# Kernel optimization log

Hardware: AMD Instinct MI355X
Metric: run time of the kernel (lower is better)

Reference implementation:

```python
import jax, jax.numpy as jnp
import numpy as np

P, B, A, NBT, NC, NTAB, G = 512, 512, 32, 40, 3, 40, 36
NA = B * A


def setup_inputs() -> dict:
    key = jax.random.key(0)
    rng = np.random.default_rng(0)
    coords = jax.random.normal(key, (P, NA, 3), dtype=jnp.float32) * 3.0
    # residue b occupies atoms [b*A, (b+1)*A)
    offsets = np.broadcast_to(np.arange(B, dtype=np.int32) * A, (P, B)).copy()
    block_type = rng.integers(0, NBT, size=(P, B)).astype(np.int32)
    # simple linear chain per pose: conn 0 = lower (prev residue), conn 1 = upper (next residue)
    inter = np.full((P, B, NC, 2), -1, dtype=np.int32)
    inter[:, 1:, 0, 0] = np.arange(B - 1, dtype=np.int32)
    inter[:, 1:, 0, 1] = 1
    inter[:, :-1, 1, 0] = np.arange(1, B, dtype=np.int32)
    inter[:, :-1, 1, 1] = 0
    down = rng.integers(0, A, size=(NBT, NC, A)).astype(np.int32)
    bt_rama_table = rng.integers(0, NTAB, size=(NBT, 2)).astype(np.int32)
    bt_upper_conn_ind = np.ones(NBT, dtype=np.int32)
    bt_is_pro = rng.integers(0, 2, size=NBT).astype(np.int32)
    # unresolved torsion atoms: (local_atom_ind, conn_ind, n_bonds_from_conn); atom_ind<0 => via connection
    tor = np.zeros((NBT, 8, 3), dtype=np.int32)
    tor[:, 0] = (-1, 0, 0)  # phi: prev-C via lower conn
    tor[:, 1] = (0, -1, 0)  # N
    tor[:, 2] = (1, -1, 0)  # CA
    tor[:, 3] = (2, -1, 0)  # C
    tor[:, 4] = (0, -1, 0)  # psi: N
    tor[:, 5] = (1, -1, 0)  # CA
    tor[:, 6] = (2, -1, 0)  # C
    tor[:, 7] = (-1, 1, 0)  # next-N via upper conn
    rama_tables = jax.random.normal(jax.random.fold_in(key, 1), (NTAB, G, G), dtype=jnp.float32)
    tp = np.zeros((NTAB, 2, 2), dtype=np.float32)
    tp[:, 0, :] = -np.pi            # bb start
    tp[:, 1, :] = 2.0 * np.pi / G   # bb step
    return dict(
        coords=coords,
        pose_stack_block_coord_offset=jnp.asarray(offsets),
        pose_stack_block_type=jnp.asarray(block_type),
        pose_stack_inter_residue_connections=jnp.asarray(inter),
        bt_atom_downstream_of_conn=jnp.asarray(down),
        bt_rama_table=jnp.asarray(bt_rama_table),
        bt_upper_conn_ind=jnp.asarray(bt_upper_conn_ind),
        bt_is_pro=jnp.asarray(bt_is_pro),
        bt_rama_torsion_atoms=jnp.asarray(tor),
        rama_tables=rama_tables,
        table_params=jnp.asarray(tp),
    )


def _dihedral(p):
    # p: [..., 4, 3] -> dihedral angle [...] via atan2 formulation
    b1 = p[..., 1, :] - p[..., 0, :]
    b2 = p[..., 2, :] - p[..., 1, :]
    b3 = p[..., 3, :] - p[..., 2, :]
    n1 = jnp.cross(b1, b2)
    n2 = jnp.cross(b2, b3)
    b2n = b2 / (jnp.linalg.norm(b2, axis=-1, keepdims=True) + 1e-12)
    m1 = jnp.cross(n1, b2n)
    x = jnp.sum(n1 * n2, axis=-1)
    y = jnp.sum(m1 * n2, axis=-1)
    return jnp.arctan2(y, x)


def _catmull_rom_w(f):
    # weights over 4 neighbors (i-1, i, i+1, i+2); f in [0,1)
    f2 = f * f
    f3 = f2 * f
    return jnp.stack(
        [0.5 * (-f3 + 2 * f2 - f), 0.5 * (3 * f3 - 5 * f2 + 2),
         0.5 * (-3 * f3 + 4 * f2 + f), 0.5 * (f3 - f2)], axis=-1)


def reference(coords, pose_stack_block_coord_offset, pose_stack_block_type,
              pose_stack_inter_residue_connections, bt_atom_downstream_of_conn,
              bt_rama_table, bt_upper_conn_ind, bt_is_pro, bt_rama_torsion_atoms,
              rama_tables, table_params):
    nP, nB = pose_stack_block_type.shape
    nG = rama_tables.shape[-1]
    pidx = jnp.arange(nP)[:, None, None]
    bidx = jnp.arange(nB)[None, :, None]
    bt = pose_stack_block_type                       # [P,B]
    tor = bt_rama_torsion_atoms[bt]                  # [P,B,8,3]
    atom_ind, conn_ind, nbonds = tor[..., 0], tor[..., 1], tor[..., 2]
    safe_conn = jnp.clip(conn_ind, 0, None)
    other_block = pose_stack_inter_residue_connections[pidx, bidx, safe_conn, 0]  # [P,B,8]
    other_conn = pose_stack_inter_residue_connections[pidx, bidx, safe_conn, 1]
    conn_ok = (conn_ind >= 0) & (other_block >= 0)
    ob = jnp.clip(other_block, 0, None)
    oc = jnp.clip(other_conn, 0, None)
    obt = bt[pidx, ob]                               # [P,B,8]
    down_atom = bt_atom_downstream_of_conn[obt, oc, nbonds]
    conn_global = pose_stack_block_coord_offset[pidx, ob] + down_atom
    local_global = pose_stack_block_coord_offset[pidx, bidx] + jnp.clip(atom_ind, 0, None)
    use_local = atom_ind >= 0
    gidx = jnp.where(use_local, local_global, conn_global)  # [P,B,8]
    atom_ok = use_local | conn_ok
    xyz = coords[pidx, gidx]                         # [P,B,8,3]
    ang = _dihedral(xyz.reshape(nP, nB, 2, 4, 3))    # [P,B,2] -> (phi, psi)
    tor_ok = jnp.all(atom_ok.reshape(nP, nB, 2, 4), axis=-1)
    # table selection: proline-dependent on the NEXT residue
    uc = bt_upper_conn_ind[bt]                       # [P,B]
    p2 = jnp.arange(nP)[:, None]
    b2 = jnp.arange(nB)[None, :]
    nb = pose_stack_inter_residue_connections[p2, b2, uc, 0]  # [P,B]
    nb_ok = nb >= 0
    nbt = bt[p2, jnp.clip(nb, 0, None)]
    tab = bt_rama_table[bt, bt_is_pro[nbt]]          # [P,B]
    start = table_params[tab, 0]                     # [P,B,2]
    step = table_params[tab, 1]
    u = (ang - start) / step                         # [P,B,2]
    i0f = jnp.floor(u)
    f = u - i0f
    i0 = i0f.astype(jnp.int32)
    offs = jnp.arange(-1, 3, dtype=jnp.int32)        # 4 spline neighbors
    ii = jnp.mod(i0[..., 0:1] + offs, nG)            # [P,B,4] periodic phi bins
    jj = jnp.mod(i0[..., 1:2] + offs, nG)            # [P,B,4] periodic psi bins
    wphi = _catmull_rom_w(f[..., 0])                 # [P,B,4]
    wpsi = _catmull_rom_w(f[..., 1])
    vals = rama_tables[tab[..., None, None], ii[..., :, None], jj[..., None, :]]  # [P,B,4,4]
    e = jnp.einsum('pbi,pbj,pbij->pb', wphi, wpsi, vals)
    ok = tor_ok[..., 0] & tor_ok[..., 1] & nb_ok
    return jnp.sum(jnp.where(ok, e, 0.0), axis=-1)   # [P] per-pose rama score
```

## Files before the change

### kernel.cpp

```cpp
#include <hip/hip_runtime.h>
#include <math.h>

#define NP 512
#define NBLK 512
#define NTHREADS 1024
#define NA_ 32
#define NCn 3
#define NG 36
#define NBT 40
#define NTAB 40

struct F3 { float x, y, z; };
__device__ inline F3 f3sub(F3 a, F3 b) { return {a.x - b.x, a.y - b.y, a.z - b.z}; }
__device__ inline F3 f3cross(F3 a, F3 b) {
    return {a.y * b.z - a.z * b.y, a.z * b.x - a.x * b.z, a.x * b.y - a.y * b.x};
}
__device__ inline float f3dot(F3 a, F3 b) { return a.x * b.x + a.y * b.y + a.z * b.z; }

__global__ __launch_bounds__(NTHREADS, 4) void rama_kernel(
    const float* __restrict__ coords,
    const int*   __restrict__ offsets,
    const int*   __restrict__ block_type,
    const int*   __restrict__ inter,
    const int*   __restrict__ down,
    const int*   __restrict__ bt_rama_table,
    const int*   __restrict__ bt_upper_conn,
    const int*   __restrict__ bt_is_pro,
    const int*   __restrict__ tor_atoms,
    const float* __restrict__ rama_tables,
    const float* __restrict__ table_params,
    float*       __restrict__ out)
{
    __shared__ __align__(16) int   s_bt[NBLK];
    __shared__ __align__(16) int   s_off[NBLK];
    __shared__ __align__(16) int   s_inter[NBLK * NCn * 2];
    __shared__ __align__(16) float s_ang[NBLK * 2];
    __shared__ float partial[NTHREADS / 64];

    const int p   = blockIdx.x;
    const int tid = threadIdx.x;

    {
        const int4* gi = (const int4*)(inter      + (size_t)p * NBLK * NCn * 2);
        const int4* gb = (const int4*)(block_type + (size_t)p * NBLK);
        const int4* go = (const int4*)(offsets    + (size_t)p * NBLK);
        if (tid < 768)      ((int4*)s_inter)[tid]     = gi[tid];
        else if (tid < 896) ((int4*)s_bt)[tid - 768]  = gb[tid - 768];
        else                ((int4*)s_off)[tid - 896] = go[tid - 896];
    }
    __syncthreads();

    const int b = tid & (NBLK - 1);
    const int t = tid >> 9;
    const int bt    = s_bt[b];
    const int off_b = s_off[b];
    const float* pose_coords = coords + (size_t)p * NBLK * NA_ * 3;

    const int4* tq = (const int4*)tor_atoms + (6 * bt + 3 * t);
    const int4 w0 = tq[0], w1 = tq[1], w2 = tq[2];
    const int ai[4]  = {w0.x, w0.w, w1.z, w2.y};
    const int ci[4]  = {w0.y, w1.x, w1.w, w2.z};
    const int nbd[4] = {w0.z, w1.y, w2.x, w2.w};

    int  g[4];
    bool ok4 = true;
    #pragma unroll
    for (int a = 0; a < 4; ++a) {
        if (ai[a] >= 0) {
            g[a] = off_b + ai[a];
        } else {
            const int sc = ci[a] > 0 ? ci[a] : 0;
            const int ib = (b * NCn + sc) * 2;
            const int ob = s_inter[ib + 0];
            const int oc = s_inter[ib + 1];
            ok4 = ok4 && (ci[a] >= 0) && (ob >= 0);
            const int obc = ob > 0 ? ob : 0;
            const int occ = oc > 0 ? oc : 0;
            const int obt = s_bt[obc];
            g[a] = s_off[obc] + down[(obt * NCn + occ) * NA_ + nbd[a]];
        }
    }

    F3 pts[4];
    bool done = false;
    if (g[2] == g[1] + 1 && g[3] == g[2] + 1 && (g[1] & 3) == 0) {
        const float* base = pose_coords + (size_t)g[1] * 3;
        const float4 q0 = ((const float4*)base)[0];
        const float4 q1 = ((const float4*)base)[1];
        const float  q2 = base[8];
        pts[1] = {q0.x, q0.y, q0.z};
        pts[2] = {q0.w, q1.x, q1.y};
        pts[3] = {q1.z, q1.w, q2};
        const float* c0 = pose_coords + (size_t)g[0] * 3;
        pts[0] = {c0[0], c0[1], c0[2]};
        done = true;
    } else if (g[1] == g[0] + 1 && g[2] == g[1] + 1 && (g[0] & 3) == 0) {
        const float* base = pose_coords + (size_t)g[0] * 3;
        const float4 q0 = ((const float4*)base)[0];
        const float4 q1 = ((const float4*)base)[1];
        const float  q2 = base[8];
        pts[0] = {q0.x, q0.y, q0.z};
        pts[1] = {q0.w, q1.x, q1.y};
        pts[2] = {q1.z, q1.w, q2};
        const float* c3 = pose_coords + (size_t)g[3] * 3;
        pts[3] = {c3[0], c3[1], c3[2]};
        done = true;
    }
    if (!done) {
        #pragma unroll
        for (int a = 0; a < 4; ++a) {
            const float* c = pose_coords + (size_t)g[a] * 3;
            pts[a] = {c[0], c[1], c[2]};
        }
    }

    const F3 d1 = f3sub(pts[1], pts[0]);
    const F3 d2 = f3sub(pts[2], pts[1]);
    const F3 d3 = f3sub(pts[3], pts[2]);
    const F3 n1 = f3cross(d1, d2);
    const F3 n2 = f3cross(d2, d3);
    const float inv = 1.0f / (sqrtf(f3dot(d2, d2)) + 1e-12f);
    const F3 b2n = {d2.x * inv, d2.y * inv, d2.z * inv};
    const F3 m1  = f3cross(n1, b2n);
    const float ang = atan2f(f3dot(m1, n2), f3dot(n1, n2));

    s_ang[b * 2 + t] = ok4 ? ang : 1e30f;
    __syncthreads();
    const float2 pp  = ((const float2*)s_ang)[b];
    const float  phi = pp.x, psi = pp.y;
    const bool   okb = fabsf(phi) < 1e29f && fabsf(psi) < 1e29f;

    const int  uc   = bt_upper_conn[bt];
    const int  nb   = s_inter[(b * NCn + uc) * 2 + 0];
    const bool nbok = nb >= 0;
    const int  nbc  = nb > 0 ? nb : 0;
    const int  tab  = bt_rama_table[bt * 2 + bt_is_pro[s_bt[nbc]]];

    float e = 0.0f;
    if (okb && nbok) {
        const float4 tp4 = ((const float4*)table_params)[tab];
        float wphi[4], wpsi[4];
        int   ii[4], jj[4];
        #pragma unroll
        for (int d = 0; d < 2; ++d) {
            const float a0    = (d == 0) ? phi   : psi;
            const float start = (d == 0) ? tp4.x : tp4.y;
            const float step  = (d == 0) ? tp4.z : tp4.w;
            const float u   = (a0 - start) / step;
            const float i0f = floorf(u);
            const float f   = u - i0f;
            const float f2 = f * f, f3v = f2 * f;
            float* w = (d == 0) ? wphi : wpsi;
            w[0] = 0.5f * (-f3v + 2.0f * f2 - f);
            w[1] = 0.5f * (3.0f * f3v - 5.0f * f2 + 2.0f);
            w[2] = 0.5f * (-3.0f * f3v + 4.0f * f2 + f);
            w[3] = 0.5f * (f3v - f2);
            int m = ((int)i0f - 1) % NG;
            if (m < 0) m += NG;
            int* idx = (d == 0) ? ii : jj;
            idx[0] = m;
            #pragma unroll
            for (int k = 1; k < 4; ++k) {
                m = (m + 1 == NG) ? 0 : m + 1;
                idx[k] = m;
            }
        }
        const int   ra = t ? ii[2]   : ii[0];
        const int   rb = t ? ii[3]   : ii[1];
        const float wa = t ? wphi[2] : wphi[0];
        const float wb = t ? wphi[3] : wphi[1];
        const float* T  = rama_tables + (size_t)tab * NG * NG;
        const float* Ta = T + ra * NG;
        const float* Tb = T + rb * NG;
        float sa = 0.0f, sb = 0.0f;
        #pragma unroll
        for (int j = 0; j < 4; ++j) {
            sa += wpsi[j] * Ta[jj[j]];
            sb += wpsi[j] * Tb[jj[j]];
        }
        e = wa * sa + wb * sb;
    }

    float v = e;
    #pragma unroll
    for (int o = 32; o > 0; o >>= 1) v += __shfl_down(v, o);
    const int wave = tid >> 6;
    const int lane = tid & 63;
    if (lane == 0) partial[wave] = v;
    __syncthreads();
    if (tid == 0) {
        float s = 0.0f;
        #pragma unroll
        for (int i = 0; i < NTHREADS / 64; ++i) s += partial[i];
        out[p] = s;
    }
}

extern "C" void kernel_launch(void* const* d_in, const int* in_sizes, int n_in,
                              void* d_out, int out_size, void* d_ws, size_t ws_size,
                              hipStream_t stream) {
    (void)in_sizes; (void)n_in; (void)out_size; (void)d_ws; (void)ws_size;
    rama_kernel<<<NP, NTHREADS, 0, stream>>>(
        (const float*)d_in[0],
        (const int*)d_in[1],
        (const int*)d_in[2],
        (const int*)d_in[3],
        (const int*)d_in[4],
        (const int*)d_in[5],
        (const int*)d_in[6],
        (const int*)d_in[7],
        (const int*)d_in[8],
        (const float*)d_in[9],
        (const float*)d_in[10],
        (float*)d_out);
}
```

Measured before the change: 175.5 us.

## Compute phi and psi in one thread per residue, drop LDS staging

Changes the kernel from two threads per residue (one per torsion) to one thread computing both phi and psi. When the torsions share atoms it reuses three contiguous backbone atoms loaded with one vector read. It removes the shared-memory staging of per-pose topology and the mid-kernel barrier, reading block types, offsets and connections straight from global memory. It replaces atan2f and the sqrt/divide with a polynomial atan2 and a hardware rsq/rcp, which trades some accuracy for fewer instructions.

```diff
diff --git a/kernel.cpp b/kernel.cpp
--- a/kernel.cpp
+++ b/kernel.cpp
@@ -3,12 +3,10 @@
 
 #define NP 512
 #define NBLK 512
-#define NTHREADS 1024
+#define NT 512
 #define NA_ 32
 #define NCn 3
 #define NG 36
-#define NBT 40
-#define NTAB 40
 
 struct F3 { float x, y, z; };
 __device__ inline F3 f3sub(F3 a, F3 b) { return {a.x - b.x, a.y - b.y, a.z - b.z}; }
@@ -17,7 +15,34 @@
 }
 __device__ inline float f3dot(F3 a, F3 b) { return a.x * b.x + a.y * b.y + a.z * b.z; }
 
-__global__ __launch_bounds__(NTHREADS, 4) void rama_kernel(
+__device__ inline float fast_atan2(float y, float x) {
+    const float ax = fabsf(x), ay = fabsf(y);
+    const float mx = fmaxf(ax, ay), mn = fminf(ax, ay);
+    const float r  = mn * __builtin_amdgcn_rcpf(fmaxf(mx, 1e-37f));
+    const float s  = r * r;
+    float p = -0.0117212f;
+    p = fmaf(p, s,  0.05265332f);
+    p = fmaf(p, s, -0.11643287f);
+    p = fmaf(p, s,  0.19354346f);
+    p = fmaf(p, s, -0.33262347f);
+    p = fmaf(p, s,  0.99997726f);
+    p = p * r;
+    p = (ay > ax) ? (1.5707963267948966f - p) : p;
+    p = (x < 0.0f) ? (3.14159265358979323f - p) : p;
+    return copysignf(p, y);
+}
+
+__device__ inline float dihedral4(F3 p0, F3 p1, F3 p2, F3 p3) {
+    const F3 b1 = f3sub(p1, p0);
+    const F3 b2 = f3sub(p2, p1);
+    const F3 b3 = f3sub(p3, p2);
+    const F3 n1 = f3cross(b1, b2);
+    const F3 n2 = f3cross(b2, b3);
+    const float i2 = __builtin_amdgcn_rsqf(f3dot(b2, b2) + 1e-24f);
+    return fast_atan2(i2 * f3dot(f3cross(n1, b2), n2), f3dot(n1, n2));
+}
+
+__global__ __launch_bounds__(NT, 4) void rama_kernel(
     const float* __restrict__ coords,
     const int*   __restrict__ offsets,
     const int*   __restrict__ block_type,
@@ -31,113 +56,86 @@
     const float* __restrict__ table_params,
     float*       __restrict__ out)
 {
-    __shared__ __align__(16) int   s_bt[NBLK];
-    __shared__ __align__(16) int   s_off[NBLK];
-    __shared__ __align__(16) int   s_inter[NBLK * NCn * 2];
-    __shared__ __align__(16) float s_ang[NBLK * 2];
-    __shared__ float partial[NTHREADS / 64];
-
-    const int p   = blockIdx.x;
-    const int tid = threadIdx.x;
-
-    {
-        const int4* gi = (const int4*)(inter      + (size_t)p * NBLK * NCn * 2);
-        const int4* gb = (const int4*)(block_type + (size_t)p * NBLK);
-        const int4* go = (const int4*)(offsets    + (size_t)p * NBLK);
-        if (tid < 768)      ((int4*)s_inter)[tid]     = gi[tid];
-        else if (tid < 896) ((int4*)s_bt)[tid - 768]  = gb[tid - 768];
-        else                ((int4*)s_off)[tid - 896] = go[tid - 896];
-    }
-    __syncthreads();
-
-    const int b = tid & (NBLK - 1);
-    const int t = tid >> 9;
-    const int bt    = s_bt[b];
-    const int off_b = s_off[b];
+    __shared__ float partial[NT / 64];
+
+    const int p  = blockIdx.x;
+    const int b  = threadIdx.x;
+    const int pb = p * NBLK + b;
+
+    const int bt    = block_type[pb];
+    const int off_b = offsets[pb];
     const float* pose_coords = coords + (size_t)p * NBLK * NA_ * 3;
-
-    const int4* tq = (const int4*)tor_atoms + (6 * bt + 3 * t);
-    const int4 w0 = tq[0], w1 = tq[1], w2 = tq[2];
-    const int ai[4]  = {w0.x, w0.w, w1.z, w2.y};
-    const int ci[4]  = {w0.y, w1.x, w1.w, w2.z};
-    const int nbd[4] = {w0.z, w1.y, w2.x, w2.w};
-
-    int  g[4];
-    bool ok4 = true;
+    const int*   inter_p     = inter  + (size_t)p * NBLK * NCn * 2;
+
+    const int4* tq = (const int4*)tor_atoms + 6 * bt;
+    const int4 w0 = tq[0], w1 = tq[1], w2 = tq[2], w3 = tq[3], w4 = tq[4], w5 = tq[5];
+    const int ai[8]  = {w0.x, w0.w, w1.z, w2.y,  w3.x, w3.w, w4.z, w5.y};
+    const int ci[8]  = {w0.y, w1.x, w1.w, w2.z,  w3.y, w4.x, w4.w, w5.z};
+    const int nbd[8] = {w0.z, w1.y, w2.x, w2.w,  w3.z, w4.y, w5.x, w5.w};
+
+    int  g[8];
+    bool ok_phi = true, ok_psi = true;
     #pragma unroll
-    for (int a = 0; a < 4; ++a) {
-        if (ai[a] >= 0) {
-            g[a] = off_b + ai[a];
+    for (int e = 0; e < 8; ++e) {
+        if (ai[e] >= 0) {
+            g[e] = off_b + ai[e];
         } else {
-            const int sc = ci[a] > 0 ? ci[a] : 0;
-            const int ib = (b * NCn + sc) * 2;
-            const int ob = s_inter[ib + 0];
-            const int oc = s_inter[ib + 1];
-            ok4 = ok4 && (ci[a] >= 0) && (ob >= 0);
+            const int sc = ci[e] > 0 ? ci[e] : 0;
+            const int ob = inter_p[(b * NCn + sc) * 2 + 0];
+            const int oc = inter_p[(b * NCn + sc) * 2 + 1];
+            const bool okc = (ci[e] >= 0) && (ob >= 0);
+            if (e < 4) ok_phi = ok_phi && okc; else ok_psi = ok_psi && okc;
             const int obc = ob > 0 ? ob : 0;
             const int occ = oc > 0 ? oc : 0;
-            const int obt = s_bt[obc];
-            g[a] = s_off[obc] + down[(obt * NCn + occ) * NA_ + nbd[a]];
-        }
-    }
-
-    F3 pts[4];
-    bool done = false;
-    if (g[2] == g[1] + 1 && g[3] == g[2] + 1 && (g[1] & 3) == 0) {
+            const int obt = block_type[p * NBLK + obc];
+            g[e] = offsets[p * NBLK + obc] + down[(obt * NCn + occ) * NA_ + nbd[e]];
+        }
+    }
+
+    float phi, psi;
+    const bool sh = (g[1] == g[4]) && (g[2] == g[5]) && (g[3] == g[6]);
+    if (sh && g[2] == g[1] + 1 && g[3] == g[1] + 2 && ((g[1] & 3) == 0)) {
         const float* base = pose_coords + (size_t)g[1] * 3;
         const float4 q0 = ((const float4*)base)[0];
         const float4 q1 = ((const float4*)base)[1];
-        const float  q2 = base[8];
-        pts[1] = {q0.x, q0.y, q0.z};
-        pts[2] = {q0.w, q1.x, q1.y};
-        pts[3] = {q1.z, q1.w, q2};
+        const float  f8 = base[8];
+        const F3 P1 = {q0.x, q0.y, q0.z};
+        const F3 P2 = {q0.w, q1.x, q1.y};
+        const F3 P3 = {q1.z, q1.w, f8};
         const float* c0 = pose_coords + (size_t)g[0] * 3;
-        pts[0] = {c0[0], c0[1], c0[2]};
-        done = true;
-    } else if (g[1] == g[0] + 1 && g[2] == g[1] + 1 && (g[0] & 3) == 0) {
-        const float* base = pose_coords + (size_t)g[0] * 3;
-        const float4 q0 = ((const float4*)base)[0];
-        const float4 q1 = ((const float4*)base)[1];
-        const float  q2 = base[8];
-        pts[0] = {q0.x, q0.y, q0.z};
-        pts[1] = {q0.w, q1.x, q1.y};
-        pts[2] = {q1.z, q1.w, q2};
-        const float* c3 = pose_coords + (size_t)g[3] * 3;
-        pts[3] = {c3[0], c3[1], c3[2]};
-        done = true;
-    }
-    if (!done) {
-        #pragma unroll
-        for (int a = 0; a < 4; ++a) {
-            const float* c = pose_coords + (size_t)g[a] * 3;
-            pts[a] = {c[0], c[1], c[2]};
-        }
-    }
-
-    const F3 d1 = f3sub(pts[1], pts[0]);
-    const F3 d2 = f3sub(pts[2], pts[1]);
-    const F3 d3 = f3sub(pts[3], pts[2]);
-    const F3 n1 = f3cross(d1, d2);
-    const F3 n2 = f3cross(d2, d3);
-    const float inv = 1.0f / (sqrtf(f3dot(d2, d2)) + 1e-12f);
-    const F3 b2n = {d2.x * inv, d2.y * inv, d2.z * inv};
-    const F3 m1  = f3cross(n1, b2n);
-    const float ang = atan2f(f3dot(m1, n2), f3dot(n1, n2));
-
-    s_ang[b * 2 + t] = ok4 ? ang : 1e30f;
-    __syncthreads();
-    const float2 pp  = ((const float2*)s_ang)[b];
-    const float  phi = pp.x, psi = pp.y;
-    const bool   okb = fabsf(phi) < 1e29f && fabsf(psi) < 1e29f;
+        const float* c7 = pose_coords + (size_t)g[7] * 3;
+        const F3 P0 = {c0[0], c0[1], c0[2]};
+        const F3 P4 = {c7[0], c7[1], c7[2]};
+        const F3 b1 = f3sub(P1, P0);
+        const F3 b2 = f3sub(P2, P1);
+        const F3 b3 = f3sub(P3, P2);
+        const F3 b4 = f3sub(P4, P3);
+        const F3 n1 = f3cross(b1, b2);
+        const F3 n2 = f3cross(b2, b3);
+        const F3 n3 = f3cross(b3, b4);
+        const float i2 = __builtin_amdgcn_rsqf(f3dot(b2, b2) + 1e-24f);
+        const float i3 = __builtin_amdgcn_rsqf(f3dot(b3, b3) + 1e-24f);
+        phi = fast_atan2(i2 * f3dot(f3cross(n1, b2), n2), f3dot(n1, n2));
+        psi = fast_atan2(i3 * f3dot(f3cross(n2, b3), n3), f3dot(n2, n3));
+    } else {
+        F3 q[8];
+        #pragma unroll
+        for (int e = 0; e < 8; ++e) {
+            const float* c = pose_coords + (size_t)g[e] * 3;
+            q[e] = {c[0], c[1], c[2]};
+        }
+        phi = dihedral4(q[0], q[1], q[2], q[3]);
+        psi = dihedral4(q[4], q[5], q[6], q[7]);
+    }
 
     const int  uc   = bt_upper_conn[bt];
-    const int  nb   = s_inter[(b * NCn + uc) * 2 + 0];
+    const int  nb   = inter_p[(b * NCn + uc) * 2 + 0];
     const bool nbok = nb >= 0;
     const int  nbc  = nb > 0 ? nb : 0;
-    const int  tab  = bt_rama_table[bt * 2 + bt_is_pro[s_bt[nbc]]];
+    const int  tab  = bt_rama_table[bt * 2 + bt_is_pro[block_type[p * NBLK + nbc]]];
 
     float e = 0.0f;
-    if (okb && nbok) {
+    if (ok_phi && ok_psi && nbok) {
         const float4 tp4 = ((const float4*)table_params)[tab];
         float wphi[4], wpsi[4];
         int   ii[4], jj[4];
@@ -165,33 +163,28 @@
                 idx[k] = m;
             }
         }
-        const int   ra = t ? ii[2]   : ii[0];
-        const int   rb = t ? ii[3]   : ii[1];
-        const float wa = t ? wphi[2] : wphi[0];
-        const float wb = t ? wphi[3] : wphi[1];
-        const float* T  = rama_tables + (size_t)tab * NG * NG;
-        const float* Ta = T + ra * NG;
-        const float* Tb = T + rb * NG;
-        float sa = 0.0f, sb = 0.0f;
-        #pragma unroll
-        for (int j = 0; j < 4; ++j) {
-            sa += wpsi[j] * Ta[jj[j]];
-            sb += wpsi[j] * Tb[jj[j]];
-        }
-        e = wa * sa + wb * sb;
+        const float* T = rama_tables + (size_t)tab * NG * NG;
+        #pragma unroll
+        for (int i = 0; i < 4; ++i) {
+            const float* Tr = T + ii[i] * NG;
+            float rs = 0.0f;
+            #pragma unroll
+            for (int j = 0; j < 4; ++j) rs += wpsi[j] * Tr[jj[j]];
+            e += wphi[i] * rs;
+        }
     }
 
     float v = e;
     #pragma unroll
     for (int o = 32; o > 0; o >>= 1) v += __shfl_down(v, o);
-    const int wave = tid >> 6;
-    const int lane = tid & 63;
+    const int wave = threadIdx.x >> 6;
+    const int lane = threadIdx.x & 63;
     if (lane == 0) partial[wave] = v;
     __syncthreads();
-    if (tid == 0) {
+    if (threadIdx.x == 0) {
         float s = 0.0f;
         #pragma unroll
-        for (int i = 0; i < NTHREADS / 64; ++i) s += partial[i];
+        for (int i = 0; i < NT / 64; ++i) s += partial[i];
         out[p] = s;
     }
 }
@@ -200,7 +193,7 @@
                               void* d_out, int out_size, void* d_ws, size_t ws_size,
                               hipStream_t stream) {
     (void)in_sizes; (void)n_in; (void)out_size; (void)d_ws; (void)ws_size;
-    rama_kernel<<<NP, NTHREADS, 0, stream>>>(
+    rama_kernel<<<NP, NT, 0, stream>>>(
         (const float*)d_in[0],
         (const int*)d_in[1],
         (const int*)d_in[2],
```

New measurement: 173.5 us. Within noise of the previous version (-1.2%).
